# Optimization experiments

Measured on AMD Instinct MI355X. Metric: run time of the kernel, lower is better.

Reference implementation:

```python
import jax, jax.numpy as jnp
import numpy as np

NB = 56  # numblock
EPS = 1e-5


def layer_norm(x, w, b):
    mu = jnp.mean(x, axis=-1, keepdims=True)
    var = jnp.mean(jnp.square(x - mu), axis=-1, keepdims=True)
    return (x - mu) * jax.lax.rsqrt(var + EPS) * w + b


def min_gru(x, w_hg, w_out):
    # lucidrains minGRU, log-space Heinsen parallel scan (seq_len > 1 branch)
    hg = x @ w_hg                      # [n, L, 2*di]
    hidden, gate = jnp.split(hg, 2, axis=-1)
    log_coeffs = -jax.nn.softplus(gate)        # log(1 - z)
    log_z = -jax.nn.softplus(-gate)            # log z
    # log_g(hidden): where(h>=0, log(relu(h)+0.5), -softplus(-h))
    log_tilde_h = jnp.where(hidden >= 0,
                            jnp.log(jax.nn.relu(hidden) + 0.5),
                            -jax.nn.softplus(-hidden))
    log_values = log_z + log_tilde_h
    a_star = jnp.cumsum(log_coeffs, axis=1)
    log_h = a_star + jax.lax.cumlogsumexp(log_values - a_star, axis=1)
    return jnp.exp(log_h) @ w_out      # [n, L, dim]


def block_fwd(x, norm_w, norm_b, dw_w, dw_b, gru1_whg, gru1_wout,
              gru2_whg, gru2_wout, norm2_w, norm2_b, p1_w, p1_b, p2_w, p2_b):
    n, L, dim = x.shape
    residual = x
    h = layer_norm(x, norm_w, norm_b)
    # depthwise 3x3 conv on [n, dim, NB, NB]
    img = h.reshape(n, NB, NB, dim).transpose(0, 3, 1, 2)
    img = jax.lax.conv_general_dilated(
        img, dw_w, window_strides=(1, 1), padding='SAME',
        feature_group_count=dim,
        dimension_numbers=('NCHW', 'OIHW', 'NCHW')) + dw_b[None, :, None, None]
    h = img.reshape(n, dim, L).transpose(0, 2, 1)
    # bidirectional minGRU: second branch on 2D-flipped sequence
    h2 = jnp.flip(h.reshape(n, NB, NB, dim), axis=(1, 2)).reshape(n, L, dim)
    x1 = min_gru(h, gru1_whg, gru1_wout)
    x2 = jnp.flip(min_gru(h2, gru2_whg, gru2_wout), axis=1)
    h = x1 + x2 + residual
    residual = h
    m = layer_norm(h, norm2_w, norm2_b)
    m = jax.nn.gelu(m @ p1_w + p1_b, approximate=False)
    m = m @ p2_w + p2_b
    return m + residual


def setup_inputs():
    key = jax.random.key(0)
    ks = jax.random.split(key, 9)
    n, dim = 16, 384
    di = 2 * dim          # expansion_factor=2
    mlp = 4 * dim         # mlp_ratio=4
    L = NB * NB

    def w(k, shape, s=0.02):
        return jax.random.normal(k, shape, jnp.float32) * s

    return {
        'x': jax.random.normal(ks[0], (n, L, dim), jnp.float32),
        'norm_w': jnp.ones((dim,), jnp.float32),
        'norm_b': jnp.zeros((dim,), jnp.float32),
        'dw_w': w(ks[1], (dim, 1, 3, 3), 0.1),
        'dw_b': jnp.zeros((dim,), jnp.float32),
        'gru1_whg': w(ks[2], (dim, 2 * di)),
        'gru1_wout': w(ks[3], (di, dim)),
        'gru2_whg': w(ks[4], (dim, 2 * di)),
        'gru2_wout': w(ks[5], (di, dim)),
        'norm2_w': jnp.ones((dim,), jnp.float32),
        'norm2_b': jnp.zeros((dim,), jnp.float32),
        'p1_w': w(ks[6], (dim, mlp)),
        'p1_b': jnp.zeros((mlp,), jnp.float32),
        'p2_w': w(ks[7], (mlp, dim)),
        'p2_b': jnp.zeros((dim,), jnp.float32),
    }


def reference(x, norm_w, norm_b, dw_w, dw_b, gru1_whg, gru1_wout,
              gru2_whg, gru2_wout, norm2_w, norm2_b, p1_w, p1_b, p2_w, p2_b):
    return block_fwd(x, norm_w, norm_b, dw_w, dw_b, gru1_whg, gru1_wout,
                     gru2_whg, gru2_wout, norm2_w, norm2_b, p1_w, p1_b, p2_w, p2_b)
```

## Files before the change

### kernel.cpp

```cpp
#include <hip/hip_runtime.h>
#include <hip/hip_bf16.h>

typedef __hip_bfloat16 bf16;
typedef __attribute__((ext_vector_type(8))) short short8;
typedef __attribute__((ext_vector_type(4))) short short4v;
typedef __attribute__((ext_vector_type(4))) float floatx4;

#define N_BATCH 16
#define NBQ 56
#define SEQ (NBQ*NBQ)
#define DIM 384
#define DI 768
#define MROWS (N_BATCH*SEQ)
#define NSEG 49
#define SEGLEN 64

__device__ __forceinline__ float b2f(bf16 v){ return __bfloat162float(v); }
__device__ __forceinline__ bf16 f2b(float v){ return __float2bfloat16(v); }

__device__ __forceinline__ float ldin(const void* p, size_t i, int f32){
    return f32 ? ((const float*)p)[i] : __bfloat162float(((const bf16*)p)[i]);
}
__device__ __forceinline__ void stout(void* p, size_t i, int f32, float v){
    if (f32) ((float*)p)[i] = v; else ((bf16*)p)[i] = __float2bfloat16(v);
}

__device__ __forceinline__ void gl2lds16(const void* g, void* l) {
    __builtin_amdgcn_global_load_lds((const __attribute__((address_space(1))) void*)g,
                                     (__attribute__((address_space(3))) void*)l, 16, 0, 0);
}

__global__ void detect_kernel(const unsigned short* __restrict__ x, int* __restrict__ flag) {
    __shared__ int cnt;
    if (threadIdx.x == 0) cnt = 0;
    __syncthreads();
    int c = 0;
    for (int i = threadIdx.x; i < 16384; i += 256) {
        unsigned short u = x[i];
        if ((u & 0x7F80) == 0x7F80) ++c;
    }
    if (c) atomicAdd(&cnt, c);
    __syncthreads();
    if (threadIdx.x == 0) *flag = cnt ? 1 : 0;
}

__global__ __launch_bounds__(64) void ln_kernel(const void* __restrict__ x,
        const void* __restrict__ w, const void* __restrict__ b,
        bf16* __restrict__ y, size_t row_off, const int* __restrict__ flag) {
    const int f32 = *flag;
    const size_t row = row_off + blockIdx.x;
    const int lane = threadIdx.x;
    float v[6]; float s = 0.f;
    #pragma unroll
    for (int j = 0; j < 6; ++j) { v[j] = ldin(x, row*DIM + lane + j*64, f32); s += v[j]; }
    #pragma unroll
    for (int o = 32; o; o >>= 1) s += __shfl_xor(s, o);
    const float mu = s * (1.f/DIM);
    float s2 = 0.f;
    #pragma unroll
    for (int j = 0; j < 6; ++j) { float d = v[j]-mu; s2 += d*d; }
    #pragma unroll
    for (int o = 32; o; o >>= 1) s2 += __shfl_xor(s2, o);
    const float inv = rsqrtf(s2*(1.f/DIM) + 1e-5f);
    bf16* yr = y + (size_t)blockIdx.x * DIM;
    #pragma unroll
    for (int j = 0; j < 6; ++j) {
        int c = lane + j*64;
        yr[c] = f2b((v[j]-mu)*inv*ldin(w, c, f32) + ldin(b, c, f32));
    }
}

__device__ __forceinline__ floatx4 ld_tok4(const bf16* p){
    short4v s = *(const short4v*)p;
    floatx4 f;
    #pragma unroll
    for (int k = 0; k < 4; ++k) {
        unsigned int u = ((unsigned int)(unsigned short)s[k]) << 16;
        f[k] = __uint_as_float(u);
    }
    return f;
}

__global__ __launch_bounds__(192) void dwconv_kernel(const bf16* __restrict__ h,
        const void* __restrict__ w, const void* __restrict__ bias,
        bf16* __restrict__ out, const int* __restrict__ flag) {
    const int f32 = *flag;
    const int tid = threadIdx.x;
    const int c4  = tid % 96;
    const int j   = blockIdx.x*2 + tid/96;
    const int i0  = blockIdx.y*8;
    const int n   = blockIdx.z;
    const int c0  = c4*4;
    const bf16* hn = h + (size_t)n*SEQ*DIM + c0;

    floatx4 wgt[9];
    #pragma unroll
    for (int t = 0; t < 9; ++t)
        #pragma unroll
        for (int k = 0; k < 4; ++k)
            wgt[t][k] = ldin(w, (size_t)(c0+k)*9 + t, f32);
    floatx4 bv;
    #pragma unroll
    for (int k = 0; k < 4; ++k) bv[k] = ldin(bias, c0+k, f32);

    const floatx4 zero = (floatx4){0.f,0.f,0.f,0.f};
    floatx4 win[3][3];
    #pragma unroll
    for (int dj = 0; dj < 3; ++dj) {
        const int jj = j + dj - 1;
        const bool jok = (unsigned)jj < NBQ;
        win[0][dj] = (jok && i0 > 0) ? ld_tok4(hn + ((size_t)((i0-1)*NBQ + jj))*DIM) : zero;
        win[1][dj] =  jok            ? ld_tok4(hn + ((size_t)( i0   *NBQ + jj))*DIM) : zero;
    }
    bf16* on = out + (size_t)n*SEQ*DIM + c0;
    #pragma unroll
    for (int r = 0; r < 8; ++r) {
        const int i = i0 + r;
        #pragma unroll
        for (int dj = 0; dj < 3; ++dj) {
            const int jj = j + dj - 1;
            const bool ok = ((unsigned)jj < NBQ) && (i+1 < NBQ);
            win[2][dj] = ok ? ld_tok4(hn + ((size_t)((i+1)*NBQ + jj))*DIM) : zero;
        }
        floatx4 acc = bv;
        #pragma unroll
        for (int di = 0; di < 3; ++di)
            #pragma unroll
            for (int dj = 0; dj < 3; ++dj)
                #pragma unroll
                for (int k = 0; k < 4; ++k)
                    acc[k] += win[di][dj][k] * wgt[di*3+dj][k];
        short4v o;
        #pragma unroll
        for (int k = 0; k < 4; ++k) { bf16 t = f2b(acc[k]); o[k] = *(short*)&t; }
        *(short4v*)(on + ((size_t)(i*NBQ + j))*DIM) = o;
        #pragma unroll
        for (int dj = 0; dj < 3; ++dj) { win[0][dj] = win[1][dj]; win[1][dj] = win[2][dj]; }
    }
}

__global__ __launch_bounds__(64) void scan_p1(const bf16* __restrict__ G,
        float* __restrict__ Aseg, float* __restrict__ Bseg, int dir) {
    const int c = blockIdx.x*64 + threadIdx.x;
    const int s = blockIdx.y;
    const int n = blockIdx.z;
    const bf16* base = G + (size_t)n*SEQ*(2*DI) + c;
    float A = 1.f, B = 0.f;
    #pragma unroll 4
    for (int u = 0; u < SEGLEN; ++u) {
        const int t = dir ? (SEQ-1 - (s*SEGLEN + u)) : (s*SEGLEN + u);
        const bf16* p = base + (size_t)t*(2*DI);
        float hid = b2f(p[0]), gate = b2f(p[DI]);
        float z  = 1.f/(1.f + __expf(-gate));
        float tl = hid >= 0.f ? hid + 0.5f : 1.f/(1.f + __expf(-hid));
        float a = 1.f - z;
        A *= a;
        B = a*B + z*tl;
    }
    const size_t idx = ((size_t)n*NSEG + s)*DI + c;
    Aseg[idx] = A; Bseg[idx] = B;
}

__global__ __launch_bounds__(64) void scan_p2(const float* __restrict__ Aseg,
        const float* __restrict__ Bseg, float* __restrict__ Pseg) {
    const int c = blockIdx.x*64 + threadIdx.x;
    const int n = blockIdx.y;
    float P = 0.f;
    for (int s = 0; s < NSEG; ++s) {
        const size_t idx = ((size_t)n*NSEG + s)*DI + c;
        Pseg[idx] = P;
        P = Aseg[idx]*P + Bseg[idx];
    }
}

__global__ __launch_bounds__(64) void scan_p3(bf16* __restrict__ G,
        const float* __restrict__ Pseg, int dir) {
    const int c = blockIdx.x*64 + threadIdx.x;
    const int s = blockIdx.y;
    const int n = blockIdx.z;
    bf16* base = G + (size_t)n*SEQ*(2*DI) + c;
    float h = Pseg[((size_t)n*NSEG + s)*DI + c];
    #pragma unroll 4
    for (int u = 0; u < SEGLEN; ++u) {
        const int t = dir ? (SEQ-1 - (s*SEGLEN + u)) : (s*SEGLEN + u);
        bf16* p = base + (size_t)t*(2*DI);
        float hid = b2f(p[0]), gate = b2f(p[DI]);
        float z  = 1.f/(1.f + __expf(-gate));
        float tl = hid >= 0.f ? hid + 0.5f : 1.f/(1.f + __expf(-hid));
        h = (1.f - z)*h + z*tl;
        p[0] = f2b(h);
    }
}

__global__ void transpose_kernel(const void* __restrict__ src, bf16* __restrict__ dst,
                                 int R, int C, const int* __restrict__ flag) {
    const int f32 = *flag;
    int idx = blockIdx.x*256 + threadIdx.x;
    if (idx >= R*C) return;
    int r = idx / C, c = idx - r*C;
    dst[(size_t)c*R + r] = f2b(ldin(src, idx, f32));
}

template<int MODE>
__global__ __launch_bounds__(256, 2) void gemm_kernel(
        const bf16* __restrict__ A, int lda,
        const bf16* __restrict__ Bt,
        void* __restrict__ C, int ldc, int K, size_t row_off,
        const void* __restrict__ bias, const void* __restrict__ resid,
        const int* __restrict__ flag) {
    __shared__ __align__(16) short lsA[128*64];
    __shared__ __align__(16) short lsB[128*64];
    const int tid  = threadIdx.x;

    const int nwg = gridDim.x * gridDim.y;
    int bid = blockIdx.y * gridDim.x + blockIdx.x;
    {
        const int q = nwg >> 3, r = nwg & 7;
        const int xcd = bid & 7, ix = bid >> 3;
        bid = (xcd < r ? xcd*(q+1) : r*(q+1) + (xcd-r)*q) + ix;
    }
    const int tn0  = (bid % gridDim.x) * 128;
    const int tm0  = (bid / gridDim.x) * 128;

    const int lane = tid & 63;
    const int wave = tid >> 6;
    const int wm = (wave & 1) * 64;
    const int wn = (wave >> 1) * 64;
    const int row16 = lane & 15;
    const int quad  = lane >> 4;
    const int r7    = row16 & 7;

    floatx4 acc[4][4];
    #pragma unroll
    for (int i = 0; i < 4; ++i)
        #pragma unroll
        for (int j = 0; j < 4; ++j)
            acc[i][j] = (floatx4){0.f, 0.f, 0.f, 0.f};

    const int so_row = tid >> 3;
    const int so_pb  = tid & 7;
    const int so_lb  = so_pb ^ (so_row & 7);

    for (int k0 = 0; k0 < K; k0 += 64) {
        const char* Ab = (const char*)(A + (size_t)tm0*lda + k0);
        const char* Bb = (const char*)(Bt + (size_t)tn0*K + k0);
        #pragma unroll
        for (int it = 0; it < 4; ++it) {
            int row = it*32 + so_row;
            gl2lds16(Ab + (size_t)row*((size_t)lda*2) + so_lb*16,
                     (char*)lsA + row*128 + so_pb*16);
        }
        #pragma unroll
        for (int it = 0; it < 4; ++it) {
            int row = it*32 + so_row;
            gl2lds16(Bb + (size_t)row*((size_t)K*2) + so_lb*16,
                     (char*)lsB + row*128 + so_pb*16);
        }
        __syncthreads();
        #pragma unroll
        for (int kk = 0; kk < 64; kk += 32) {
            const int lb = (kk >> 3) + quad;
            const int pb = (lb ^ r7) * 8;
            short8 af[4], bfr[4];
            #pragma unroll
            for (int i = 0; i < 4; ++i)
                af[i] = *(const short8*)(lsA + (wm + i*16 + row16)*64 + pb);
            #pragma unroll
            for (int j = 0; j < 4; ++j)
                bfr[j] = *(const short8*)(lsB + (wn + j*16 + row16)*64 + pb);
            #pragma unroll
            for (int i = 0; i < 4; ++i)
                #pragma unroll
                for (int j = 0; j < 4; ++j)
                    acc[i][j] = __builtin_amdgcn_mfma_f32_16x16x32_bf16(af[i], bfr[j], acc[i][j], 0, 0, 0);
        }
        __syncthreads();
    }

    const int f32 = (MODE == 0) ? 0 : *flag;
    #pragma unroll
    for (int i = 0; i < 4; ++i) {
        #pragma unroll
        for (int j = 0; j < 4; ++j) {
            #pragma unroll
            for (int r = 0; r < 4; ++r) {
                const int gm = tm0 + wm + i*16 + quad*4 + r;
                const int gn = tn0 + wn + j*16 + row16;
                float v = acc[i][j][r];
                if (MODE == 0) {
                    ((bf16*)C)[(size_t)gm*ldc + gn] = f2b(v);
                } else if (MODE == 1) {
                    size_t gi = (row_off + gm)*(size_t)ldc + gn;
                    v += ldin(resid, gi, f32);
                    stout(C, gi, f32, v);
                } else if (MODE == 2) {
                    v += ldin(bias, gn, f32);
                    v = 0.5f*v*(1.f + erff(v*0.70710678118f));
                    ((bf16*)C)[(size_t)gm*ldc + gn] = f2b(v);
                } else {
                    size_t gi = (row_off + gm)*(size_t)ldc + gn;
                    v += ldin(bias, gn, f32) + ldin(resid, gi, f32);
                    stout(C, gi, f32, v);
                }
            }
        }
    }
}

extern "C" void kernel_launch(void* const* d_in, const int* in_sizes, int n_in,
                              void* d_out, int out_size, void* d_ws, size_t ws_size,
                              hipStream_t stream) {
    const void* x       = d_in[0];
    const void* norm_w  = d_in[1];
    const void* norm_b  = d_in[2];
    const void* dw_w    = d_in[3];
    const void* dw_b    = d_in[4];
    const void* whg1    = d_in[5];
    const void* wout1   = d_in[6];
    const void* whg2    = d_in[7];
    const void* wout2   = d_in[8];
    const void* norm2_w = d_in[9];
    const void* norm2_b = d_in[10];
    const void* p1_w    = d_in[11];
    const void* p1_b    = d_in[12];
    const void* p2_w    = d_in[13];
    const void* p2_b    = d_in[14];
    void* out = d_out;
    char* ws = (char*)d_ws;

    const size_t WSZ = 5898240;

    int CH = 16;
    for (;;) {
        size_t need = 256 + WSZ + (size_t)CH * SEQ * 4608;
        if (need <= ws_size || CH == 2) break;
        CH >>= 1;
    }
    const int NC = N_BATCH / CH;
    const int CHROWS = CH * SEQ;

    int* flag = (int*)ws;
    char* wb = ws + 256;
    bf16* WhgT1  = (bf16*)(wb);
    bf16* WhgT2  = (bf16*)(wb + 1179648);
    bf16* WoutT1 = (bf16*)(wb + 2359296);
    bf16* WoutT2 = (bf16*)(wb + 2949120);
    bf16* P1T    = (bf16*)(wb + 3538944);
    bf16* P2T    = (bf16*)(wb + 4718592);
    char* dyn = ws + 256 + WSZ;
    bf16* h_ln_c   = (bf16*)(dyn);
    bf16* h_conv_c = (bf16*)(dyn + (size_t)CHROWS*DIM*2);
    bf16* Gbuf     = (bf16*)(dyn + 2*(size_t)CHROWS*DIM*2);
    bf16* mid_ln_c = h_ln_c;
    float* Aseg = (float*)h_ln_c;
    float* Bseg = Aseg + (size_t)CH*NSEG*DI;
    float* Pseg = Bseg + (size_t)CH*NSEG*DI;

    detect_kernel<<<1, 256, 0, stream>>>((const unsigned short*)x, flag);

    transpose_kernel<<<(384*1536+255)/256, 256, 0, stream>>>(whg1, WhgT1, 384, 1536, flag);
    transpose_kernel<<<(384*1536+255)/256, 256, 0, stream>>>(whg2, WhgT2, 384, 1536, flag);
    transpose_kernel<<<(768*384+255)/256, 256, 0, stream>>>(wout1, WoutT1, 768, 384, flag);
    transpose_kernel<<<(768*384+255)/256, 256, 0, stream>>>(wout2, WoutT2, 768, 384, flag);
    transpose_kernel<<<(384*1536+255)/256, 256, 0, stream>>>(p1_w, P1T, 384, 1536, flag);
    transpose_kernel<<<(1536*384+255)/256, 256, 0, stream>>>(p2_w, P2T, 1536, 384, flag);

    for (int pass = 0; pass < 2; ++pass) {
        const bf16* WhgT  = pass ? WhgT2  : WhgT1;
        const bf16* WoutT = pass ? WoutT2 : WoutT1;
        for (int ck = 0; ck < NC; ++ck) {
            const size_t roff = (size_t)ck * CHROWS;
            if (pass == 0 || NC > 1) {
                ln_kernel<<<CHROWS, 64, 0, stream>>>(x, norm_w, norm_b, h_ln_c, roff, flag);
                dwconv_kernel<<<dim3(28, 7, CH), 192, 0, stream>>>(h_ln_c, dw_w, dw_b, h_conv_c, flag);
            }
            gemm_kernel<0><<<dim3(1536/128, CHROWS/128), 256, 0, stream>>>(
                h_conv_c, DIM, WhgT, Gbuf, 2*DI, DIM, 0, nullptr, nullptr, flag);
            scan_p1<<<dim3(12, NSEG, CH), 64, 0, stream>>>(Gbuf, Aseg, Bseg, pass);
            scan_p2<<<dim3(12, CH), 64, 0, stream>>>(Aseg, Bseg, Pseg);
            scan_p3<<<dim3(12, NSEG, CH), 64, 0, stream>>>(Gbuf, Pseg, pass);
            const void* resid = pass ? (const void*)out : x;
            gemm_kernel<1><<<dim3(DIM/128, CHROWS/128), 256, 0, stream>>>(
                Gbuf, 2*DI, WoutT, out, DIM, DI, roff, nullptr, resid, flag);
        }
    }

    for (int ck = 0; ck < NC; ++ck) {
        const size_t roff = (size_t)ck * CHROWS;
        ln_kernel<<<CHROWS, 64, 0, stream>>>(out, norm2_w, norm2_b, mid_ln_c, roff, flag);
        gemm_kernel<2><<<dim3(1536/128, CHROWS/128), 256, 0, stream>>>(
            mid_ln_c, DIM, P1T, Gbuf, 1536, DIM, 0, p1_b, nullptr, flag);
        gemm_kernel<3><<<dim3(DIM/128, CHROWS/128), 256, 0, stream>>>(
            Gbuf, 1536, P2T, out, DIM, 1536, roff, p2_b, out, flag);
    }
}
```

Baseline: 1.129 ms.

## Add 256x256-tile MFMA GEMM with XCD-aware block remap for wide projections

Adds a new GEMM kernel with 256x256 output tiles, 512 threads (8 waves each computing 128x64), double-buffered direct global-to-LDS loads with XOR swizzle, and a block-index remap that groups neighbouring tiles on the same XCD. It is used for the two N=1536 projections (GRU hidden/gate and MLP up-projection with GELU) when the row count divides by 256. The aim is more data reuse per tile and better L2 locality. In exchange it uses 128 KB of LDS per block and many accumulator registers, which limits occupancy. The epilogue also writes scalar bf16 values, which may be uncoalesced.

```diff
diff --git a/kernel.cpp b/kernel.cpp
--- a/kernel.cpp
+++ b/kernel.cpp
@@ -307,6 +307,113 @@
     }
 }
 
+template<int MODE>
+__global__ __launch_bounds__(512, 2) void gemm256_kernel(
+        const bf16* __restrict__ A, int lda,
+        const bf16* __restrict__ Bt,
+        bf16* __restrict__ C, int ldc, int K,
+        const void* __restrict__ bias, const int* __restrict__ flag) {
+    __shared__ __align__(16) short lsA[2][256*64];
+    __shared__ __align__(16) short lsB[2][256*64];
+    const int tid  = threadIdx.x;
+
+    const int nwg = gridDim.x * gridDim.y;
+    int bid = blockIdx.y * gridDim.x + blockIdx.x;
+    {
+        const int q = nwg >> 3, r = nwg & 7;
+        const int xcd = bid & 7, ix = bid >> 3;
+        bid = (xcd < r ? xcd*(q+1) : r*(q+1) + (xcd-r)*q) + ix;
+    }
+    const int tn0  = (bid % gridDim.x) * 256;
+    const int tm0  = (bid / gridDim.x) * 256;
+
+    const int lane = tid & 63;
+    const int wave = tid >> 6;
+    const int wm = (wave & 1) * 128;
+    const int wn = (wave >> 1) * 64;
+    const int row16 = lane & 15;
+    const int quad  = lane >> 4;
+    const int r7    = row16 & 7;
+
+    floatx4 acc[8][4];
+    #pragma unroll
+    for (int i = 0; i < 8; ++i)
+        #pragma unroll
+        for (int j = 0; j < 4; ++j)
+            acc[i][j] = (floatx4){0.f, 0.f, 0.f, 0.f};
+
+    const int so_row = tid >> 3;
+    const int so_pb  = tid & 7;
+    const int so_lb  = so_pb ^ (so_row & 7);
+    const size_t lda2 = (size_t)lda * 2;
+    const size_t ldb2 = (size_t)K * 2;
+    const char* aSrc[4]; const char* bSrc[4];
+    #pragma unroll
+    for (int it = 0; it < 4; ++it) {
+        aSrc[it] = (const char*)A + (size_t)(tm0 + it*64 + so_row)*lda2 + so_lb*16;
+        bSrc[it] = (const char*)Bt + (size_t)(tn0 + it*64 + so_row)*ldb2 + so_lb*16;
+    }
+
+    auto stage = [&](short* dA, short* dB, int t) {
+        const int toff = t*128;
+        #pragma unroll
+        for (int it = 0; it < 4; ++it) {
+            gl2lds16(aSrc[it] + toff, (char*)dA + it*8192 + tid*16);
+            gl2lds16(bSrc[it] + toff, (char*)dB + it*8192 + tid*16);
+        }
+    };
+
+    auto compute = [&](const short* la, const short* lb_) {
+        #pragma unroll
+        for (int kk = 0; kk < 64; kk += 32) {
+            const int pb = (((kk >> 3) + quad) ^ r7) * 8;
+            short8 af[8], bfr[4];
+            #pragma unroll
+            for (int i = 0; i < 8; ++i)
+                af[i] = *(const short8*)(la + (wm + i*16 + row16)*64 + pb);
+            #pragma unroll
+            for (int j = 0; j < 4; ++j)
+                bfr[j] = *(const short8*)(lb_ + (wn + j*16 + row16)*64 + pb);
+            #pragma unroll
+            for (int i = 0; i < 8; ++i)
+                #pragma unroll
+                for (int j = 0; j < 4; ++j)
+                    acc[i][j] = __builtin_amdgcn_mfma_f32_16x16x32_bf16(af[i], bfr[j], acc[i][j], 0, 0, 0);
+        }
+    };
+
+    const int nt = K >> 6;
+    stage(lsA[0], lsB[0], 0);
+    __syncthreads();
+    for (int t = 0; t < nt; t += 2) {
+        if (t + 1 < nt) stage(lsA[1], lsB[1], t + 1);
+        compute(lsA[0], lsB[0]);
+        __syncthreads();
+        if (t + 2 < nt) stage(lsA[0], lsB[0], t + 2);
+        compute(lsA[1], lsB[1]);
+        __syncthreads();
+    }
+
+    const int f32 = (MODE == 0) ? 0 : *flag;
+    #pragma unroll
+    for (int i = 0; i < 8; ++i) {
+        #pragma unroll
+        for (int j = 0; j < 4; ++j) {
+            #pragma unroll
+            for (int r = 0; r < 4; ++r) {
+                const int gm = tm0 + wm + i*16 + quad*4 + r;
+                const int gn = tn0 + wn + j*16 + row16;
+                float v = acc[i][j][r];
+                if (MODE == 2) {
+                    v += ldin(bias, gn, f32);
+                    v = 0.5f*v*(1.f + erff(v*0.70710678118f));
+                }
+                C[(size_t)gm*ldc + gn] = f2b(v);
+            }
+        }
+    }
+}
+
 extern "C" void kernel_launch(void* const* d_in, const int* in_sizes, int n_in,
                               void* d_out, int out_size, void* d_ws, size_t ws_size,
                               hipStream_t stream) {
@@ -338,6 +445,7 @@
     }
     const int NC = N_BATCH / CH;
     const int CHROWS = CH * SEQ;
+    const bool big256 = (CHROWS % 256) == 0;
 
     int* flag = (int*)ws;
     char* wb = ws + 256;
@@ -374,8 +482,12 @@
                 ln_kernel<<<CHROWS, 64, 0, stream>>>(x, norm_w, norm_b, h_ln_c, roff, flag);
                 dwconv_kernel<<<dim3(28, 7, CH), 192, 0, stream>>>(h_ln_c, dw_w, dw_b, h_conv_c, flag);
             }
-            gemm_kernel<0><<<dim3(1536/128, CHROWS/128), 256, 0, stream>>>(
-                h_conv_c, DIM, WhgT, Gbuf, 2*DI, DIM, 0, nullptr, nullptr, flag);
+            if (big256)
+                gemm256_kernel<0><<<dim3(1536/256, CHROWS/256), 512, 0, stream>>>(
+                    h_conv_c, DIM, WhgT, Gbuf, 2*DI, DIM, nullptr, flag);
+            else
+                gemm_kernel<0><<<dim3(1536/128, CHROWS/128), 256, 0, stream>>>(
+                    h_conv_c, DIM, WhgT, Gbuf, 2*DI, DIM, 0, nullptr, nullptr, flag);
             scan_p1<<<dim3(12, NSEG, CH), 64, 0, stream>>>(Gbuf, Aseg, Bseg, pass);
             scan_p2<<<dim3(12, CH), 64, 0, stream>>>(Aseg, Bseg, Pseg);
             scan_p3<<<dim3(12, NSEG, CH), 64, 0, stream>>>(Gbuf, Pseg, pass);
@@ -388,8 +500,12 @@
     for (int ck = 0; ck < NC; ++ck) {
         const size_t roff = (size_t)ck * CHROWS;
         ln_kernel<<<CHROWS, 64, 0, stream>>>(out, norm2_w, norm2_b, mid_ln_c, roff, flag);
-        gemm_kernel<2><<<dim3(1536/128, CHROWS/128), 256, 0, stream>>>(
-            mid_ln_c, DIM, P1T, Gbuf, 1536, DIM, 0, p1_b, nullptr, flag);
+        if (big256)
+            gemm256_kernel<2><<<dim3(1536/256, CHROWS/256), 512, 0, stream>>>(
+                mid_ln_c, DIM, P1T, Gbuf, 1536, DIM, p1_b, flag);
+        else
+            gemm_kernel<2><<<dim3(1536/128, CHROWS/128), 256, 0, stream>>>(
+                mid_ln_c, DIM, P1T, Gbuf, 1536, DIM, 0, p1_b, nullptr, flag);
         gemm_kernel<3><<<dim3(DIM/128, CHROWS/128), 256, 0, stream>>>(
             Gbuf, 1536, P2T, out, DIM, 1536, roff, p2_b, out, flag);
     }
```

Result: slower. 1.248 ms (+10.5%).

## Merge both GRU input projections into one wide GEMM; widen LN and scan blocks

Applied to the files above, without the earlier changes.

When the workspace allows, the two minGRU input projections run as one 3072-wide GEMM. It relies on the two transposed weight matrices sitting next to each other in memory, and the output goes to a double-width G buffer that both scan directions read with a row stride parameter. This removes a separate GEMM pass and any repeated LayerNorm or depthwise-conv work, at the cost of a larger per-chunk workspace. LayerNorm and the three scan kernels also move from 64-thread to 256-thread blocks, which cuts block count and scheduling overhead.

```diff
diff --git a/kernel.cpp b/kernel.cpp
--- a/kernel.cpp
+++ b/kernel.cpp
@@ -44,12 +44,14 @@
     if (threadIdx.x == 0) *flag = cnt ? 1 : 0;
 }
 
-__global__ __launch_bounds__(64) void ln_kernel(const void* __restrict__ x,
+__global__ __launch_bounds__(256) void ln_kernel(const void* __restrict__ x,
         const void* __restrict__ w, const void* __restrict__ b,
         bf16* __restrict__ y, size_t row_off, const int* __restrict__ flag) {
     const int f32 = *flag;
-    const size_t row = row_off + blockIdx.x;
-    const int lane = threadIdx.x;
+    const int lane = threadIdx.x & 63;
+    const int wrow = threadIdx.x >> 6;
+    const size_t lrow = (size_t)blockIdx.x*4 + wrow;
+    const size_t row  = row_off + lrow;
     float v[6]; float s = 0.f;
     #pragma unroll
     for (int j = 0; j < 6; ++j) { v[j] = ldin(x, row*DIM + lane + j*64, f32); s += v[j]; }
@@ -62,7 +64,7 @@
     #pragma unroll
     for (int o = 32; o; o >>= 1) s2 += __shfl_xor(s2, o);
     const float inv = rsqrtf(s2*(1.f/DIM) + 1e-5f);
-    bf16* yr = y + (size_t)blockIdx.x * DIM;
+    bf16* yr = y + lrow * DIM;
     #pragma unroll
     for (int j = 0; j < 6; ++j) {
         int c = lane + j*64;
@@ -139,17 +141,17 @@
     }
 }
 
-__global__ __launch_bounds__(64) void scan_p1(const bf16* __restrict__ G,
+__global__ __launch_bounds__(256) void scan_p1(const bf16* __restrict__ G, int ldg,
         float* __restrict__ Aseg, float* __restrict__ Bseg, int dir) {
-    const int c = blockIdx.x*64 + threadIdx.x;
+    const int c = blockIdx.x*256 + threadIdx.x;
     const int s = blockIdx.y;
     const int n = blockIdx.z;
-    const bf16* base = G + (size_t)n*SEQ*(2*DI) + c;
+    const bf16* base = G + (size_t)n*SEQ*ldg + c;
     float A = 1.f, B = 0.f;
     #pragma unroll 4
     for (int u = 0; u < SEGLEN; ++u) {
         const int t = dir ? (SEQ-1 - (s*SEGLEN + u)) : (s*SEGLEN + u);
-        const bf16* p = base + (size_t)t*(2*DI);
+        const bf16* p = base + (size_t)t*ldg;
         float hid = b2f(p[0]), gate = b2f(p[DI]);
         float z  = 1.f/(1.f + __expf(-gate));
         float tl = hid >= 0.f ? hid + 0.5f : 1.f/(1.f + __expf(-hid));
@@ -161,9 +163,9 @@
     Aseg[idx] = A; Bseg[idx] = B;
 }
 
-__global__ __launch_bounds__(64) void scan_p2(const float* __restrict__ Aseg,
+__global__ __launch_bounds__(256) void scan_p2(const float* __restrict__ Aseg,
         const float* __restrict__ Bseg, float* __restrict__ Pseg) {
-    const int c = blockIdx.x*64 + threadIdx.x;
+    const int c = blockIdx.x*256 + threadIdx.x;
     const int n = blockIdx.y;
     float P = 0.f;
     for (int s = 0; s < NSEG; ++s) {
@@ -173,17 +175,17 @@
     }
 }
 
-__global__ __launch_bounds__(64) void scan_p3(bf16* __restrict__ G,
+__global__ __launch_bounds__(256) void scan_p3(bf16* __restrict__ G, int ldg,
         const float* __restrict__ Pseg, int dir) {
-    const int c = blockIdx.x*64 + threadIdx.x;
+    const int c = blockIdx.x*256 + threadIdx.x;
     const int s = blockIdx.y;
     const int n = blockIdx.z;
-    bf16* base = G + (size_t)n*SEQ*(2*DI) + c;
+    bf16* base = G + (size_t)n*SEQ*ldg + c;
     float h = Pseg[((size_t)n*NSEG + s)*DI + c];
     #pragma unroll 4
     for (int u = 0; u < SEGLEN; ++u) {
         const int t = dir ? (SEQ-1 - (s*SEGLEN + u)) : (s*SEGLEN + u);
-        bf16* p = base + (size_t)t*(2*DI);
+        bf16* p = base + (size_t)t*ldg;
         float hid = b2f(p[0]), gate = b2f(p[DI]);
         float z  = 1.f/(1.f + __expf(-gate));
         float tl = hid >= 0.f ? hid + 0.5f : 1.f/(1.f + __expf(-hid));
@@ -330,14 +332,17 @@
 
     const size_t WSZ = 5898240;
 
+    const bool merged = (256 + WSZ + (size_t)2*SEQ*7680 <= ws_size);
+    const size_t perCH = merged ? 7680 : 4608;
     int CH = 16;
     for (;;) {
-        size_t need = 256 + WSZ + (size_t)CH * SEQ * 4608;
+        size_t need = 256 + WSZ + (size_t)CH * SEQ * perCH;
         if (need <= ws_size || CH == 2) break;
         CH >>= 1;
     }
     const int NC = N_BATCH / CH;
     const int CHROWS = CH * SEQ;
+    const int GW = merged ? 3072 : 1536;
 
     int* flag = (int*)ws;
     char* wb = ws + 256;
@@ -365,29 +370,48 @@
     transpose_kernel<<<(384*1536+255)/256, 256, 0, stream>>>(p1_w, P1T, 384, 1536, flag);
     transpose_kernel<<<(1536*384+255)/256, 256, 0, stream>>>(p2_w, P2T, 1536, 384, flag);
 
-    for (int pass = 0; pass < 2; ++pass) {
-        const bf16* WhgT  = pass ? WhgT2  : WhgT1;
-        const bf16* WoutT = pass ? WoutT2 : WoutT1;
+    if (merged) {
         for (int ck = 0; ck < NC; ++ck) {
             const size_t roff = (size_t)ck * CHROWS;
-            if (pass == 0 || NC > 1) {
-                ln_kernel<<<CHROWS, 64, 0, stream>>>(x, norm_w, norm_b, h_ln_c, roff, flag);
-                dwconv_kernel<<<dim3(28, 7, CH), 192, 0, stream>>>(h_ln_c, dw_w, dw_b, h_conv_c, flag);
+            ln_kernel<<<CHROWS/4, 256, 0, stream>>>(x, norm_w, norm_b, h_ln_c, roff, flag);
+            dwconv_kernel<<<dim3(28, 7, CH), 192, 0, stream>>>(h_ln_c, dw_w, dw_b, h_conv_c, flag);
+            gemm_kernel<0><<<dim3(3072/128, CHROWS/128), 256, 0, stream>>>(
+                h_conv_c, DIM, WhgT1, Gbuf, GW, DIM, 0, nullptr, nullptr, flag);
+            for (int pass = 0; pass < 2; ++pass) {
+                bf16* Gm = Gbuf + pass*1536;
+                scan_p1<<<dim3(3, NSEG, CH), 256, 0, stream>>>(Gm, GW, Aseg, Bseg, pass);
+                scan_p2<<<dim3(3, CH), 256, 0, stream>>>(Aseg, Bseg, Pseg);
+                scan_p3<<<dim3(3, NSEG, CH), 256, 0, stream>>>(Gm, GW, Pseg, pass);
+                const void* resid = pass ? (const void*)out : x;
+                gemm_kernel<1><<<dim3(DIM/128, CHROWS/128), 256, 0, stream>>>(
+                    Gm, GW, pass ? WoutT2 : WoutT1, out, DIM, DI, roff, nullptr, resid, flag);
             }
-            gemm_kernel<0><<<dim3(1536/128, CHROWS/128), 256, 0, stream>>>(
-                h_conv_c, DIM, WhgT, Gbuf, 2*DI, DIM, 0, nullptr, nullptr, flag);
-            scan_p1<<<dim3(12, NSEG, CH), 64, 0, stream>>>(Gbuf, Aseg, Bseg, pass);
-            scan_p2<<<dim3(12, CH), 64, 0, stream>>>(Aseg, Bseg, Pseg);
-            scan_p3<<<dim3(12, NSEG, CH), 64, 0, stream>>>(Gbuf, Pseg, pass);
-            const void* resid = pass ? (const void*)out : x;
-            gemm_kernel<1><<<dim3(DIM/128, CHROWS/128), 256, 0, stream>>>(
-                Gbuf, 2*DI, WoutT, out, DIM, DI, roff, nullptr, resid, flag);
+        }
+    } else {
+        for (int pass = 0; pass < 2; ++pass) {
+            const bf16* WhgT  = pass ? WhgT2  : WhgT1;
+            const bf16* WoutT = pass ? WoutT2 : WoutT1;
+            for (int ck = 0; ck < NC; ++ck) {
+                const size_t roff = (size_t)ck * CHROWS;
+                if (pass == 0 || NC > 1) {
+                    ln_kernel<<<CHROWS/4, 256, 0, stream>>>(x, norm_w, norm_b, h_ln_c, roff, flag);
+                    dwconv_kernel<<<dim3(28, 7, CH), 192, 0, stream>>>(h_ln_c, dw_w, dw_b, h_conv_c, flag);
+                }
+                gemm_kernel<0><<<dim3(1536/128, CHROWS/128), 256, 0, stream>>>(
+                    h_conv_c, DIM, WhgT, Gbuf, GW, DIM, 0, nullptr, nullptr, flag);
+                scan_p1<<<dim3(3, NSEG, CH), 256, 0, stream>>>(Gbuf, GW, Aseg, Bseg, pass);
+                scan_p2<<<dim3(3, CH), 256, 0, stream>>>(Aseg, Bseg, Pseg);
+                scan_p3<<<dim3(3, NSEG, CH), 256, 0, stream>>>(Gbuf, GW, Pseg, pass);
+                const void* resid = pass ? (const void*)out : x;
+                gemm_kernel<1><<<dim3(DIM/128, CHROWS/128), 256, 0, stream>>>(
+                    Gbuf, GW, WoutT, out, DIM, DI, roff, nullptr, resid, flag);
+            }
         }
     }
 
     for (int ck = 0; ck < NC; ++ck) {
         const size_t roff = (size_t)ck * CHROWS;
-        ln_kernel<<<CHROWS, 64, 0, stream>>>(out, norm2_w, norm2_b, mid_ln_c, roff, flag);
+        ln_kernel<<<CHROWS/4, 256, 0, stream>>>(out, norm2_w, norm2_b, mid_ln_c, roff, flag);
         gemm_kernel<2><<<dim3(1536/128, CHROWS/128), 256, 0, stream>>>(
             mid_ln_c, DIM, P1T, Gbuf, 1536, DIM, 0, p1_b, nullptr, flag);
         gemm_kernel<3><<<dim3(DIM/128, CHROWS/128), 256, 0, stream>>>(
```

Result: slower. 1.252 ms (+10.9%).
